# Kernel tuning notes

Hardware: AMD Instinct MI355X
Metric: run time of the kernel (lower is better)

Reference implementation:

```python
import jax, jax.numpy as jnp
import numpy as np

N_NODES = 100000
N_HYPEREDGES = 20000
N_INC = 1600000
NFEAT = 256
NCLASS = 64

def setup_inputs() -> dict:
    key = jax.random.key(0)
    k1, k2, k3, k4 = jax.random.split(key, 4)
    x = jax.random.normal(k1, (N_NODES, NFEAT), dtype=jnp.float32)
    node_idx = jax.random.randint(k2, (N_INC,), 0, N_NODES)
    edge_idx = jax.random.randint(k3, (N_INC,), 0, N_HYPEREDGES)
    adj = jnp.stack([node_idx, edge_idx], axis=0)  # [2, N_INC] hyperedge incidence list
    W = jax.random.normal(k4, (NFEAT, NCLASS), dtype=jnp.float32) / np.sqrt(NFEAT).astype(np.float32)
    b = jnp.zeros((NCLASS,), dtype=jnp.float32)
    return {"x": x, "adj": adj, "W": W, "b": b}

def reference(x, adj, W, b):
    # HypergraphConv: out = D^{-1} H B^{-1} H^T (x W) + b, then ReLU
    node_idx = adj[0]  # [E] node index of each incidence
    edge_idx = adj[1]  # [E] hyperedge index of each incidence
    xw = x @ W  # [N, C]

    ones = jnp.ones(node_idx.shape[0], dtype=xw.dtype)
    D = jax.ops.segment_sum(ones, node_idx, num_segments=N_NODES)        # node degree
    Dinv = jnp.where(D > 0, 1.0 / D, 0.0)
    B = jax.ops.segment_sum(ones, edge_idx, num_segments=N_HYPEREDGES)   # hyperedge degree
    Binv = jnp.where(B > 0, 1.0 / B, 0.0)

    # node -> hyperedge aggregation, normalized by B^{-1}
    e_feat = jax.ops.segment_sum(xw[node_idx], edge_idx, num_segments=N_HYPEREDGES) * Binv[:, None]
    # hyperedge -> node aggregation, normalized by D^{-1}
    out = jax.ops.segment_sum(e_feat[edge_idx], node_idx, num_segments=N_NODES) * Dinv[:, None]
    out = out + b
    return jax.nn.relu(out)
```

## Files before the change

kernel.cpp:

```cpp
#include <hip/hip_runtime.h>

#define N_NODES 100000
#define N_EDGES 20000
#define N_INC   1600000
#define NFEAT   256
#define NCLASS  64

#define ELOC 2500
#define NLOC 12500
#define BCAP 201728
#define EPB  8
#define LCAP 192

typedef int v4i __attribute__((ext_vector_type(4)));

__global__ __launch_bounds__(256) void k_bucket(const int* __restrict__ nidx,
                                                const int* __restrict__ eidx,
                                                unsigned int* __restrict__ ebkt,
                                                unsigned int* __restrict__ nbkt,
                                                int* __restrict__ bcur) {
    __shared__ unsigned int stage[16][LCAP];
    __shared__ int lcnt[16];
    __shared__ int gbase[16];
    const int t = threadIdx.x;
    if (t < 16) lcnt[t] = 0;
    __syncthreads();

    const int base = blockIdx.x * 1024 + t * 4;
    if (base < N_INC) {
        const v4i e4 = __builtin_nontemporal_load((const v4i*)&eidx[base]);
        const v4i n4 = __builtin_nontemporal_load((const v4i*)&nidx[base]);
        const int es[4] = {e4.x, e4.y, e4.z, e4.w};
        const int ns[4] = {n4.x, n4.y, n4.z, n4.w};
        #pragma unroll
        for (int q = 0; q < 4; ++q) {
            const int e = es[q], n = ns[q];
            {
                const int b = e & 7;
                const unsigned int pay = ((unsigned int)n << 12) | (unsigned int)(e >> 3);
                const int pos = atomicAdd(&lcnt[b], 1);
                if (pos < LCAP) stage[b][pos] = pay;
                else ebkt[(size_t)b * BCAP + atomicAdd(&bcur[b], 1)] = pay;
            }
            {
                const int b = 8 + (n & 7);
                const unsigned int pay = ((unsigned int)e << 14) | (unsigned int)(n >> 3);
                const int pos = atomicAdd(&lcnt[b], 1);
                if (pos < LCAP) stage[b][pos] = pay;
                else nbkt[(size_t)(b - 8) * BCAP + atomicAdd(&bcur[b], 1)] = pay;
            }
        }
    }
    __syncthreads();
    if (t < 16) gbase[t] = atomicAdd(&bcur[t], min(lcnt[t], LCAP));
    __syncthreads();
    #pragma unroll 1
    for (int k = 0; k < 16; ++k) {
        const int cnt = min(lcnt[k], LCAP);
        const int gb  = gbase[k];
        unsigned int* dst = (k < 8) ? &ebkt[(size_t)k * BCAP]
                                    : &nbkt[(size_t)(k - 8) * BCAP];
        for (int i = t; i < cnt; i += 256) dst[gb + i] = stage[k][i];
    }
}

__global__ __launch_bounds__(256) void k_hist(const unsigned int* __restrict__ bkt,
                                              const int* __restrict__ bcur,
                                              int cur_off,
                                              unsigned short* __restrict__ hist,
                                              int SZ, unsigned int mask) {
    extern __shared__ unsigned int h[];
    const int r = blockIdx.x & 7, b = blockIdx.x >> 3;
    const int t = threadIdx.x;
    for (int i = t; i < SZ; i += 256) h[i] = 0;
    __syncthreads();
    const int cnt = bcur[cur_off + r];
    const int sz  = (cnt + EPB - 1) / EPB;
    const int lo  = b * sz, hi = min(lo + sz, cnt);
    const unsigned int* B = &bkt[(size_t)r * BCAP];
    for (int i = lo + t; i < hi; i += 256)
        atomicAdd(&h[B[i] & mask], 1u);
    __syncthreads();
    unsigned short* H = &hist[(size_t)(r * EPB + b) * SZ];
    for (int i = t; i < SZ; i += 256) H[i] = (unsigned short)h[i];
}

__global__ __launch_bounds__(256) void k_colscan(unsigned short* __restrict__ hist,
                                                 int* __restrict__ cnt_perm, int SZ) {
    const int g = blockIdx.x * 256 + threadIdx.x;
    if (g >= 8 * SZ) return;
    const int r = g / SZ, i = g - r * SZ;
    unsigned short* H = hist + (size_t)r * EPB * SZ + i;
    unsigned int run = 0;
    #pragma unroll
    for (int b = 0; b < EPB; ++b) {
        const unsigned int v = H[(size_t)b * SZ];
        H[(size_t)b * SZ] = (unsigned short)run;
        run += v;
    }
    cnt_perm[g] = (int)run;
}

__global__ __launch_bounds__(1024) void k_scan(const int* __restrict__ cnt,
                                               int* __restrict__ off, int n) {
    __shared__ int part[1024];
    const int t = threadIdx.x;
    const int chunk = ((n / 4 + 1023) / 1024) * 4;
    const int lo = min(t * chunk, n);
    const int hi = min(lo + chunk, n);
    int s = 0;
    for (int i = lo; i < hi; i += 4) {
        const int4 v = *(const int4*)&cnt[i];
        s += v.x + v.y + v.z + v.w;
    }
    part[t] = s;
    __syncthreads();
    for (int d = 1; d < 1024; d <<= 1) {
        int v = (t >= d) ? part[t - d] : 0;
        __syncthreads();
        part[t] += v;
        __syncthreads();
    }
    int run = (t == 0) ? 0 : part[t - 1];
    for (int i = lo; i < hi; i += 4) {
        const int4 v = *(const int4*)&cnt[i];
        int4 o;
        o.x = run; run += v.x;
        o.y = run; run += v.y;
        o.z = run; run += v.z;
        o.w = run; run += v.w;
        *(int4*)&off[i] = o;
    }
}

__global__ __launch_bounds__(256) void k_fill3n(const unsigned int* __restrict__ nbkt,
                                                const int* __restrict__ bcur,
                                                const unsigned short* __restrict__ nhist,
                                                const int* __restrict__ noff,
                                                unsigned short* __restrict__ ninc) {
    __shared__ unsigned int lb[NLOC];
    const int r = blockIdx.x & 7, b = blockIdx.x >> 3;
    const int t = threadIdx.x;
    const unsigned short* H = &nhist[(size_t)(r * EPB + b) * NLOC];
    const int* O = &noff[r * NLOC];
    for (int i = t; i < NLOC; i += 256) lb[i] = (unsigned int)O[i] + H[i];
    __syncthreads();
    const int cnt = bcur[8 + r];
    const int sz  = (cnt + EPB - 1) / EPB;
    const int lo  = b * sz, hi = min(lo + sz, cnt);
    const unsigned int* B = &nbkt[(size_t)r * BCAP];
    for (int i = lo + t; i < hi; i += 256) {
        const unsigned int u = B[i];
        const unsigned int pos = atomicAdd(&lb[u & 0x3FFFu], 1u);
        ninc[pos] = (unsigned short)(u >> 14);
    }
}

__global__ __launch_bounds__(256) void k_fill3e(const unsigned int* __restrict__ ebkt,
                                                const int* __restrict__ bcur,
                                                const unsigned short* __restrict__ ehist,
                                                const int* __restrict__ eoff,
                                                int* __restrict__ einc) {
    __shared__ unsigned int lb[ELOC];
    const int r = blockIdx.x & 7, b = blockIdx.x >> 3;
    const int t = threadIdx.x;
    const unsigned short* H = &ehist[(size_t)(r * EPB + b) * ELOC];
    const int* O = &eoff[r * ELOC];
    for (int i = t; i < ELOC; i += 256) lb[i] = (unsigned int)O[i] + H[i];
    __syncthreads();
    const int cnt = bcur[r];
    const int sz  = (cnt + EPB - 1) / EPB;
    const int lo  = b * sz, hi = min(lo + sz, cnt);
    const unsigned int* B = &ebkt[(size_t)r * BCAP];
    for (int i = lo + t; i < hi; i += 256) {
        const unsigned int u = B[i];
        const unsigned int pos = atomicAdd(&lb[u & 0xFFFu], 1u);
        einc[pos] = (int)(u >> 12);
    }
}

__global__ __launch_bounds__(256) void k_gemm(const float* __restrict__ x,
                                              const float* __restrict__ W,
                                              float* __restrict__ xw) {
    __shared__ float xs[64][68];
    __shared__ float wt[64][64];
    const int t  = threadIdx.x;
    const int tr = t >> 4;
    const int tc = t & 15;
    const int block_row = blockIdx.x * 64;

    float acc[4][4] = {};

    for (int k0 = 0; k0 < NFEAT; k0 += 64) {
        {
            const int rr = t >> 2;
            const int q  = t & 3;
            const int grow = block_row + rr;
            #pragma unroll
            for (int it = 0; it < 4; ++it) {
                const int kk = q * 4 + it * 16;
                float4 v = make_float4(0.f, 0.f, 0.f, 0.f);
                if (grow < N_NODES)
                    v = *(const float4*)&x[(size_t)grow * NFEAT + k0 + kk];
                xs[kk + 0][rr] = v.x;
                xs[kk + 1][rr] = v.y;
                xs[kk + 2][rr] = v.z;
                xs[kk + 3][rr] = v.w;
            }
        }
        {
            #pragma unroll
            for (int it = 0; it < 4; ++it) {
                const int k = tr + it * 16;
                *(float4*)&wt[k][tc * 4] =
                    *(const float4*)&W[(size_t)(k0 + k) * NCLASS + tc * 4];
            }
        }
        __syncthreads();

        #pragma unroll 16
        for (int kk = 0; kk < 64; ++kk) {
            const float4 xv = *(const float4*)&xs[kk][tr * 4];
            const float4 wv = *(const float4*)&wt[kk][tc * 4];
            const float xa[4] = {xv.x, xv.y, xv.z, xv.w};
            const float wa[4] = {wv.x, wv.y, wv.z, wv.w};
            #pragma unroll
            for (int i2 = 0; i2 < 4; ++i2)
                #pragma unroll
                for (int j2 = 0; j2 < 4; ++j2)
                    acc[i2][j2] = fmaf(xa[i2], wa[j2], acc[i2][j2]);
        }
        __syncthreads();
    }

    #pragma unroll
    for (int i2 = 0; i2 < 4; ++i2) {
        const int r = block_row + tr * 4 + i2;
        if (r < N_NODES) {
            float4 v = make_float4(acc[i2][0], acc[i2][1], acc[i2][2], acc[i2][3]);
            *(float4*)&xw[(size_t)r * NCLASS + tc * 4] = v;
        }
    }
}

__global__ __launch_bounds__(256) void k_edge_gather(const int* __restrict__ einc,
                                                     const int* __restrict__ eoff,
                                                     const int* __restrict__ ecnt,
                                                     const float* __restrict__ xw,
                                                     float* __restrict__ e_feat) {
    const int wave = (blockIdx.x * 256 + threadIdx.x) >> 6;
    const int lane = threadIdx.x & 63;
    if (wave >= N_EDGES) return;
    const int idx  = (wave & 7) * ELOC + (wave >> 3);
    const int base = eoff[idx];
    const int deg  = ecnt[idx];
    float a0 = 0.f, a1 = 0.f, a2 = 0.f, a3 = 0.f;
    int j = base;
    const int end = base + deg;
    for (; j + 4 <= end; j += 4) {
        const int n0 = einc[j], n1 = einc[j + 1], n2 = einc[j + 2], n3 = einc[j + 3];
        a0 += xw[(size_t)n0 * NCLASS + lane];
        a1 += xw[(size_t)n1 * NCLASS + lane];
        a2 += xw[(size_t)n2 * NCLASS + lane];
        a3 += xw[(size_t)n3 * NCLASS + lane];
    }
    for (; j < end; ++j) a0 += xw[(size_t)einc[j] * NCLASS + lane];
    const float s = (a0 + a1) + (a2 + a3);
    e_feat[(size_t)wave * NCLASS + lane] = (deg > 0) ? s / (float)deg : 0.f;
}

__global__ __launch_bounds__(256) void k_node_gather(const unsigned short* __restrict__ ninc,
                                                     const int* __restrict__ noff,
                                                     const int* __restrict__ ncnt,
                                                     const float* __restrict__ e_feat,
                                                     const float* __restrict__ b,
                                                     float* __restrict__ out) {
    const int wave = (blockIdx.x * 256 + threadIdx.x) >> 6;
    const int lane = threadIdx.x & 63;
    if (wave >= N_NODES) return;
    const int idx  = (wave & 7) * NLOC + (wave >> 3);
    const int base = noff[idx];
    const int deg  = ncnt[idx];
    float a0 = 0.f, a1 = 0.f, a2 = 0.f, a3 = 0.f;
    int j = base;
    const int end = base + deg;
    for (; j + 4 <= end; j += 4) {
        const int e0 = ninc[j], e1 = ninc[j + 1], e2 = ninc[j + 2], e3 = ninc[j + 3];
        a0 += e_feat[(size_t)e0 * NCLASS + lane];
        a1 += e_feat[(size_t)e1 * NCLASS + lane];
        a2 += e_feat[(size_t)e2 * NCLASS + lane];
        a3 += e_feat[(size_t)e3 * NCLASS + lane];
    }
    for (; j < end; ++j) a0 += e_feat[(size_t)ninc[j] * NCLASS + lane];
    const float s = (a0 + a1) + (a2 + a3);
    const float r = (deg > 0) ? s / (float)deg : 0.f;
    out[(size_t)wave * NCLASS + lane] = fmaxf(r + b[lane], 0.f);
}

extern "C" void kernel_launch(void* const* d_in, const int* in_sizes, int n_in,
                              void* d_out, int out_size, void* d_ws, size_t ws_size,
                              hipStream_t stream) {
    const float* x    = (const float*)d_in[0];
    const int*   adj  = (const int*)d_in[1];
    const float* W    = (const float*)d_in[2];
    const float* bias = (const float*)d_in[3];
    const int* nidx = adj;
    const int* eidx = adj + N_INC;
    float* out = (float*)d_out;

    char* ws = (char*)d_ws;
    unsigned int*   ebkt  = (unsigned int*)(ws);
    unsigned int*   nbkt  = (unsigned int*)(ws + 6455296);
    unsigned short* ninc  = (unsigned short*)(ws + 12910592);
    unsigned short* nhist = (unsigned short*)(ws + 16110592);
    unsigned short* ehist = (unsigned short*)(ws + 17710592);
    int* ncnt = (int*)(ws + 18030592);
    int* noff = (int*)(ws + 18430592);
    int* ecnt = (int*)(ws + 18830592);
    int* eoff = (int*)(ws + 18910592);
    int* bcur = (int*)(ws + 18990592);
    int*   einc   = (int*)(ws + 6455296);
    float* e_feat = (float*)(ws);

    hipMemsetAsync(bcur, 0, 64, stream);

    k_bucket<<<(N_INC + 1023) / 1024, 256, 0, stream>>>(nidx, eidx, ebkt, nbkt, bcur);

    k_hist<<<8 * EPB, 256, ELOC * 4, stream>>>(ebkt, bcur, 0, ehist, ELOC, 0xFFFu);
    k_hist<<<8 * EPB, 256, NLOC * 4, stream>>>(nbkt, bcur, 8, nhist, NLOC, 0x3FFFu);

    k_colscan<<<(8 * ELOC + 255) / 256, 256, 0, stream>>>(ehist, ecnt, ELOC);
    k_colscan<<<(8 * NLOC + 255) / 256, 256, 0, stream>>>(nhist, ncnt, NLOC);
    k_scan<<<1, 1024, 0, stream>>>(ecnt, eoff, N_EDGES);
    k_scan<<<1, 1024, 0, stream>>>(ncnt, noff, N_NODES);

    k_fill3n<<<8 * EPB, 256, 0, stream>>>(nbkt, bcur, nhist, noff, ninc);
    k_fill3e<<<8 * EPB, 256, 0, stream>>>(ebkt, bcur, ehist, eoff, einc);

    k_gemm<<<(N_NODES + 63) / 64, 256, 0, stream>>>(x, W, out);

    k_edge_gather<<<(N_EDGES * 64) / 256, 256, 0, stream>>>(einc, eoff, ecnt, out, e_feat);

    k_node_gather<<<(N_NODES * 64) / 256, 256, 0, stream>>>(ninc, noff, ncnt, e_feat, bias, out);
}
```

Before: 533.8 us.

## Restructure GEMM to keep all of W in LDS and stream x rows from registers

The xW GEMM kernel now loads the entire 256x64 W matrix into shared memory once per block. Each thread computes a 4x8 output tile and reads its x rows directly from global memory as float4 with one-step register prefetch, which removes the shared-memory staging of x and the per-tile barriers. Blocks now cover 128 rows. The trade-offs are 64KB of LDS per block, which limits occupancy, and uncoalesced per-thread strided x loads (eight threads share the same rows and rely on cache).

New measurement: 553.4 us. 3.7% more time.

```diff
diff --git a/kernel.cpp b/kernel.cpp
--- a/kernel.cpp
+++ b/kernel.cpp
@@ -182,63 +182,63 @@
 __global__ __launch_bounds__(256) void k_gemm(const float* __restrict__ x,
                                               const float* __restrict__ W,
                                               float* __restrict__ xw) {
-    __shared__ float xs[64][68];
-    __shared__ float wt[64][64];
-    const int t  = threadIdx.x;
-    const int tr = t >> 4;
-    const int tc = t & 15;
-    const int block_row = blockIdx.x * 64;
-
-    float acc[4][4] = {};
-
-    for (int k0 = 0; k0 < NFEAT; k0 += 64) {
-        {
-            const int rr = t >> 2;
-            const int q  = t & 3;
-            const int grow = block_row + rr;
+    __shared__ __align__(16) float Wl[NFEAT * NCLASS];
+    const int t = threadIdx.x;
+    {
+        const float4* src = (const float4*)W;
+        float4* dst = (float4*)Wl;
+        #pragma unroll
+        for (int i = 0; i < 16; ++i)
+            dst[t + i * 256] = src[t + i * 256];
+    }
+    __syncthreads();
+
+    const int rowg = t >> 3;
+    const int cg   = (t & 7) * 8;
+    const int r0   = blockIdx.x * 128 + rowg * 4;
+
+    float acc[4][8] = {};
+    float4 xa[4];
+    #pragma unroll
+    for (int i = 0; i < 4; ++i)
+        xa[i] = (r0 + i < N_NODES) ? *(const float4*)&x[(size_t)(r0 + i) * NFEAT]
+                                   : make_float4(0.f, 0.f, 0.f, 0.f);
+
+    for (int k0 = 0; k0 < NFEAT; k0 += 4) {
+        float4 xb[4];
+        const int k1 = k0 + 4;
+        #pragma unroll
+        for (int i = 0; i < 4; ++i) {
+            if (k1 < NFEAT && r0 + i < N_NODES)
+                xb[i] = *(const float4*)&x[(size_t)(r0 + i) * NFEAT + k1];
+            else
+                xb[i] = make_float4(0.f, 0.f, 0.f, 0.f);
+        }
+        #pragma unroll
+        for (int kk = 0; kk < 4; ++kk) {
+            const float4 w0 = *(const float4*)&Wl[(k0 + kk) * NCLASS + cg];
+            const float4 w1 = *(const float4*)&Wl[(k0 + kk) * NCLASS + cg + 4];
+            const float wv[8] = {w0.x, w0.y, w0.z, w0.w, w1.x, w1.y, w1.z, w1.w};
             #pragma unroll
-            for (int it = 0; it < 4; ++it) {
-                const int kk = q * 4 + it * 16;
-                float4 v = make_float4(0.f, 0.f, 0.f, 0.f);
-                if (grow < N_NODES)
-                    v = *(const float4*)&x[(size_t)grow * NFEAT + k0 + kk];
-                xs[kk + 0][rr] = v.x;
-                xs[kk + 1][rr] = v.y;
-                xs[kk + 2][rr] = v.z;
-                xs[kk + 3][rr] = v.w;
+            for (int i = 0; i < 4; ++i) {
+                const float xs1 = (kk == 0) ? xa[i].x : (kk == 1) ? xa[i].y
+                                : (kk == 2) ? xa[i].z : xa[i].w;
+                #pragma unroll
+                for (int j = 0; j < 8; ++j)
+                    acc[i][j] = fmaf(xs1, wv[j], acc[i][j]);
             }
         }
-        {
-            #pragma unroll
-            for (int it = 0; it < 4; ++it) {
-                const int k = tr + it * 16;
-                *(float4*)&wt[k][tc * 4] =
-                    *(const float4*)&W[(size_t)(k0 + k) * NCLASS + tc * 4];
-            }
-        }
-        __syncthreads();
-
-        #pragma unroll 16
-        for (int kk = 0; kk < 64; ++kk) {
-            const float4 xv = *(const float4*)&xs[kk][tr * 4];
-            const float4 wv = *(const float4*)&wt[kk][tc * 4];
-            const float xa[4] = {xv.x, xv.y, xv.z, xv.w};
-            const float wa[4] = {wv.x, wv.y, wv.z, wv.w};
-            #pragma unroll
-            for (int i2 = 0; i2 < 4; ++i2)
-                #pragma unroll
-                for (int j2 = 0; j2 < 4; ++j2)
-                    acc[i2][j2] = fmaf(xa[i2], wa[j2], acc[i2][j2]);
-        }
-        __syncthreads();
+        #pragma unroll
+        for (int i = 0; i < 4; ++i) xa[i] = xb[i];
     }
 
     #pragma unroll
-    for (int i2 = 0; i2 < 4; ++i2) {
-        const int r = block_row + tr * 4 + i2;
-        if (r < N_NODES) {
-            float4 v = make_float4(acc[i2][0], acc[i2][1], acc[i2][2], acc[i2][3]);
-            *(float4*)&xw[(size_t)r * NCLASS + tc * 4] = v;
+    for (int i = 0; i < 4; ++i) {
+        if (r0 + i < N_NODES) {
+            float4 o0 = make_float4(acc[i][0], acc[i][1], acc[i][2], acc[i][3]);
+            float4 o1 = make_float4(acc[i][4], acc[i][5], acc[i][6], acc[i][7]);
+            *(float4*)&xw[(size_t)(r0 + i) * NCLASS + cg]     = o0;
+            *(float4*)&xw[(size_t)(r0 + i) * NCLASS + cg + 4] = o1;
         }
     }
 }
@@ -337,7 +337,7 @@
     k_fill3n<<<8 * EPB, 256, 0, stream>>>(nbkt, bcur, nhist, noff, ninc);
     k_fill3e<<<8 * EPB, 256, 0, stream>>>(ebkt, bcur, ehist, eoff, einc);
 
-    k_gemm<<<(N_NODES + 63) / 64, 256, 0, stream>>>(x, W, out);
+    k_gemm<<<(N_NODES + 127) / 128, 256, 0, stream>>>(x, W, out);
 
     k_edge_gather<<<(N_EDGES * 64) / 256, 256, 0, stream>>>(einc, eoff, ecnt, out, e_feat);
 
```
